# Kernel tuning notes

Hardware: AMD Instinct MI355X
Metric: run time of the kernel (lower is better)

## Reference

```python
import jax, jax.numpy as jnp
import numpy as np

B, S, D, H = 4, 2048, 512, 8
DK = D // H
SCALE = 1.0 / np.sqrt(DK)


def setup_inputs() -> dict:
    key = jax.random.key(0)
    kx, kq, kk, kv = jax.random.split(key, 4)
    w_std = np.sqrt(2.0 / (D + D))  # xavier-ish scale
    return {
        "x": jax.random.normal(kx, (B, S, D), dtype=jnp.float32),
        "W_Q": jax.random.normal(kq, (D, D), dtype=jnp.float32) * w_std,
        "W_K": jax.random.normal(kk, (D, D), dtype=jnp.float32) * w_std,
        "W_V": jax.random.normal(kv, (D, D), dtype=jnp.float32) * w_std,
    }


def reference(x, W_Q, W_K, W_V):
    # torch Linear(bias=False): y = x @ W.T
    q = jnp.einsum('bsd,ed->bse', x, W_Q).reshape(B, S, H, DK).transpose(0, 2, 1, 3)
    k = jnp.einsum('bsd,ed->bse', x, W_K).reshape(B, S, H, DK).transpose(0, 2, 1, 3)
    v = jnp.einsum('bsd,ed->bse', x, W_V).reshape(B, S, H, DK).transpose(0, 2, 1, 3)
    scores = jnp.einsum('bhqd,bhkd->bhqk', q, k) * SCALE  # [B,H,S,S]
    scores_exp = jnp.exp(scores)  # faithful: no max-subtraction in original
    attn = scores_exp / (scores_exp.sum(axis=-1, keepdims=True) + 1e-8)
    context = jnp.einsum('bhqk,bhkd->bhqd', attn, v)
    return context.transpose(0, 2, 1, 3).reshape(B, S, D)
```

## Files before the change

### kernel.cpp

```cpp
#include <hip/hip_runtime.h>
#include <hip/hip_bf16.h>

#define Bsz 4
#define Ssz 2048
#define Dsz 512
#define Hsz 8
#define DKsz 64

typedef __bf16 bf16x8 __attribute__((ext_vector_type(8)));
typedef float f32x4 __attribute__((ext_vector_type(4)));

__global__ __launch_bounds__(256) void cvt_kernel(
    const float* __restrict__ x, const float* __restrict__ Wq,
    const float* __restrict__ Wk, const float* __restrict__ Wv,
    __bf16* __restrict__ xb, __bf16* __restrict__ Wb)
{
    const int i = blockIdx.x * 256 + threadIdx.x;
    const int XN4 = (Bsz * Ssz * Dsz) / 4;
    const float* src;
    __bf16* dst;
    int off;
    if (i < XN4) {
        src = x; dst = xb; off = i;
    } else {
        int j = i - XN4;
        int w = j >> 16;
        off = j & 65535;
        src = (w == 0) ? Wq : (w == 1) ? Wk : Wv;
        dst = Wb + (size_t)w * (Dsz * Dsz);
    }
    float4 v = ((const float4*)src)[off];
    __bf16 o[4] = {(__bf16)v.x, (__bf16)v.y, (__bf16)v.z, (__bf16)v.w};
    *(uint2*)(dst + (size_t)off * 4) = *(uint2*)o;
}

__global__ __launch_bounds__(256) void qkv_proj_kernel(
    const __bf16* __restrict__ xb, const __bf16* __restrict__ Wb,
    __bf16* __restrict__ Qo, __bf16* __restrict__ Ko, __bf16* __restrict__ Vo)
{
    __shared__ __bf16 xs[128][72];
    __shared__ __bf16 wsh[128][72];

    const int tid  = threadIdx.x;
    const int lane = tid & 63;
    const int wave = tid >> 6;
    const int quad = lane >> 4;
    const int l16  = lane & 15;
    const int wm   = (wave & 1) * 64;
    const int wn   = (wave >> 1) * 64;

    const int tm = blockIdx.x * 128;
    const int tn = blockIdx.y * 128;
    const int which = blockIdx.z;
    const __bf16* W = Wb + (size_t)which * (Dsz * Dsz);

    const int srow = tid >> 1;
    const int scol = (tid & 1) * 32;

    f32x4 acc[4][4];
    #pragma unroll
    for (int i = 0; i < 4; ++i)
        #pragma unroll
        for (int j = 0; j < 4; ++j) acc[i][j] = (f32x4){0.f, 0.f, 0.f, 0.f};

    const __bf16* xrow = xb + (size_t)(tm + srow) * Dsz + scol;
    const __bf16* wrow = W  + (size_t)(tn + srow) * Dsz + scol;

    bf16x8 px[4], pw[4];
    #pragma unroll
    for (int i = 0; i < 4; ++i) {
        px[i] = *(const bf16x8*)(xrow + 8 * i);
        pw[i] = *(const bf16x8*)(wrow + 8 * i);
    }

    const __bf16 (*Ash)[72] = (which == 2) ? wsh : xs;
    const __bf16 (*Bsh)[72] = (which == 2) ? xs : wsh;

    for (int k0 = 0; k0 < Dsz; k0 += 64) {
        __syncthreads();
        #pragma unroll
        for (int i = 0; i < 4; ++i) {
            *(bf16x8*)&xs[srow][scol + 8 * i]  = px[i];
            *(bf16x8*)&wsh[srow][scol + 8 * i] = pw[i];
        }
        __syncthreads();
        if (k0 + 64 < Dsz) {
            #pragma unroll
            for (int i = 0; i < 4; ++i) {
                px[i] = *(const bf16x8*)(xrow + k0 + 64 + 8 * i);
                pw[i] = *(const bf16x8*)(wrow + k0 + 64 + 8 * i);
            }
        }

        #pragma unroll
        for (int kk = 0; kk < 2; ++kk) {
            bf16x8 a[4], b[4];
            #pragma unroll
            for (int mi = 0; mi < 4; ++mi)
                a[mi] = *(const bf16x8*)&Ash[wm + mi * 16 + l16][kk * 32 + quad * 8];
            #pragma unroll
            for (int ni = 0; ni < 4; ++ni)
                b[ni] = *(const bf16x8*)&Bsh[wn + ni * 16 + l16][kk * 32 + quad * 8];
            #pragma unroll
            for (int mi = 0; mi < 4; ++mi)
                #pragma unroll
                for (int ni = 0; ni < 4; ++ni)
                    acc[mi][ni] = __builtin_amdgcn_mfma_f32_16x16x32_bf16(
                        a[mi], b[ni], acc[mi][ni], 0, 0, 0);
        }
    }

    const float qscale = 0.125f * 1.44269504088896340736f;

    if (which != 2) {
        #pragma unroll
        for (int ni = 0; ni < 4; ++ni) {
            const int n = tn + wn + ni * 16 + l16;
            const int h = n >> 6, d = n & 63;
            #pragma unroll
            for (int mi = 0; mi < 4; ++mi) {
                #pragma unroll
                for (int r = 0; r < 4; ++r) {
                    const int m = tm + wm + mi * 16 + quad * 4 + r;
                    const int b = m >> 11, s = m & (Ssz - 1);
                    const float v = acc[mi][ni][r];
                    if (which == 0)
                        Qo[((((size_t)b * Hsz + h) * Ssz + s) << 6) + d] = (__bf16)(v * qscale);
                    else
                        Ko[((((size_t)b * Hsz + h) * Ssz + s) << 6) + d] = (__bf16)v;
                }
            }
        }
    } else {
        #pragma unroll
        for (int mi = 0; mi < 4; ++mi) {
            #pragma unroll
            for (int r = 0; r < 4; ++r) {
                const int e = tn + wm + mi * 16 + quad * 4 + r;
                const int h = e >> 6, d = e & 63;
                #pragma unroll
                for (int ni = 0; ni < 4; ++ni) {
                    const int sx = tm + wn + ni * 16 + l16;
                    const int b = sx >> 11, s = sx & (Ssz - 1);
                    Vo[(((size_t)b * Hsz + h) * DKsz + d) * Ssz + s] = (__bf16)acc[mi][ni][r];
                }
            }
        }
    }
}

__global__ __launch_bounds__(256, 2) void attn_kernel(
    const __bf16* __restrict__ Q, const __bf16* __restrict__ K,
    const __bf16* __restrict__ VT, float* __restrict__ out)
{
    __shared__ __bf16 ks[64][72];
    __shared__ __bf16 vs[64][72];
    __shared__ __bf16 ps[4][2][16][72];

    const int tid  = threadIdx.x;
    const int lane = tid & 63;
    const int wave = tid >> 6;
    const int quad = lane >> 4;
    const int l16  = lane & 15;

    const int bh = blockIdx.x;
    const int qt = blockIdx.y;
    const int b  = bh >> 3;
    const int h  = bh & 7;

    const __bf16* Qb = Q  + (size_t)bh * Ssz * DKsz;
    const __bf16* Kb = K  + (size_t)bh * Ssz * DKsz;
    const __bf16* Vb = VT + (size_t)bh * DKsz * Ssz;

    bf16x8 qf[2][2];
    #pragma unroll
    for (int qs = 0; qs < 2; ++qs) {
        const __bf16* qrow = Qb + (size_t)(qt * 128 + qs * 64 + wave * 16 + l16) * DKsz;
        qf[qs][0] = *(const bf16x8*)(qrow + quad * 8);
        qf[qs][1] = *(const bf16x8*)(qrow + 32 + quad * 8);
    }

    bf16x8 ones;
    #pragma unroll
    for (int i = 0; i < 8; ++i) ones[i] = (__bf16)1.0f;

    f32x4 oacc[2][4];
    #pragma unroll
    for (int qs = 0; qs < 2; ++qs)
        #pragma unroll
        for (int i = 0; i < 4; ++i) oacc[qs][i] = (f32x4){0.f, 0.f, 0.f, 0.f};
    f32x4 lacc[2] = {(f32x4){0.f, 0.f, 0.f, 0.f}, (f32x4){0.f, 0.f, 0.f, 0.f}};

    const int srow = tid >> 2;
    const int sc   = (tid & 3) * 8;

    const __bf16* krow = Kb + (size_t)srow * DKsz + sc;
    const __bf16* vrow = Vb + (size_t)srow * Ssz + sc;

    bf16x8 pk0 = *(const bf16x8*)(krow);
    bf16x8 pk1 = *(const bf16x8*)(krow + 32);
    bf16x8 pv0 = *(const bf16x8*)(vrow);
    bf16x8 pv1 = *(const bf16x8*)(vrow + 32);

    for (int kb = 0; kb < Ssz; kb += 64) {
        __syncthreads();
        *(bf16x8*)&ks[srow][sc]      = pk0;
        *(bf16x8*)&ks[srow][32 + sc] = pk1;
        *(bf16x8*)&vs[srow][sc]      = pv0;
        *(bf16x8*)&vs[srow][32 + sc] = pv1;
        __syncthreads();

        if (kb + 64 < Ssz) {
            pk0 = *(const bf16x8*)(krow + (size_t)(kb + 64) * DKsz);
            pk1 = *(const bf16x8*)(krow + (size_t)(kb + 64) * DKsz + 32);
            pv0 = *(const bf16x8*)(vrow + kb + 64);
            pv1 = *(const bf16x8*)(vrow + kb + 96);
        }

        bf16x8 kf[2][4], vf[2][4];
        #pragma unroll
        for (int kk = 0; kk < 2; ++kk)
            #pragma unroll
            for (int ns = 0; ns < 4; ++ns) {
                kf[kk][ns] = *(const bf16x8*)&ks[ns * 16 + l16][kk * 32 + quad * 8];
                vf[kk][ns] = *(const bf16x8*)&vs[ns * 16 + l16][kk * 32 + quad * 8];
            }

        #pragma unroll
        for (int qs = 0; qs < 2; ++qs) {
            f32x4 sacc[4];
            #pragma unroll
            for (int ns = 0; ns < 4; ++ns) {
                sacc[ns] = (f32x4){0.f, 0.f, 0.f, 0.f};
                sacc[ns] = __builtin_amdgcn_mfma_f32_16x16x32_bf16(qf[qs][0], kf[0][ns], sacc[ns], 0, 0, 0);
                sacc[ns] = __builtin_amdgcn_mfma_f32_16x16x32_bf16(qf[qs][1], kf[1][ns], sacc[ns], 0, 0, 0);
            }
            #pragma unroll
            for (int ns = 0; ns < 4; ++ns)
                #pragma unroll
                for (int r = 0; r < 4; ++r)
                    ps[wave][qs][quad * 4 + r][ns * 16 + l16] =
                        (__bf16)__builtin_amdgcn_exp2f(sacc[ns][r]);

            bf16x8 af0 = *(const bf16x8*)&ps[wave][qs][l16][quad * 8];
            bf16x8 af1 = *(const bf16x8*)&ps[wave][qs][l16][32 + quad * 8];
            #pragma unroll
            for (int ns = 0; ns < 4; ++ns) {
                oacc[qs][ns] = __builtin_amdgcn_mfma_f32_16x16x32_bf16(af0, vf[0][ns], oacc[qs][ns], 0, 0, 0);
                oacc[qs][ns] = __builtin_amdgcn_mfma_f32_16x16x32_bf16(af1, vf[1][ns], oacc[qs][ns], 0, 0, 0);
            }
            lacc[qs] = __builtin_amdgcn_mfma_f32_16x16x32_bf16(af0, ones, lacc[qs], 0, 0, 0);
            lacc[qs] = __builtin_amdgcn_mfma_f32_16x16x32_bf16(af1, ones, lacc[qs], 0, 0, 0);
        }
    }

    #pragma unroll
    for (int qs = 0; qs < 2; ++qs) {
        float linv[4];
        #pragma unroll
        for (int r = 0; r < 4; ++r) linv[r] = 1.f / (lacc[qs][r] + 1e-8f);
        #pragma unroll
        for (int ns = 0; ns < 4; ++ns) {
            const int d = ns * 16 + l16;
            #pragma unroll
            for (int r = 0; r < 4; ++r) {
                const int s = qt * 128 + qs * 64 + wave * 16 + quad * 4 + r;
                out[((size_t)b * Ssz + s) * Dsz + h * DKsz + d] = oacc[qs][ns][r] * linv[r];
            }
        }
    }
}

extern "C" void kernel_launch(void* const* d_in, const int* in_sizes, int n_in,
                              void* d_out, int out_size, void* d_ws, size_t ws_size,
                              hipStream_t stream) {
    const float* x  = (const float*)d_in[0];
    const float* Wq = (const float*)d_in[1];
    const float* Wk = (const float*)d_in[2];
    const float* Wv = (const float*)d_in[3];
    float* out = (float*)d_out;

    const size_t per = (size_t)Bsz * Hsz * Ssz * DKsz;
    __bf16* Qw  = (__bf16*)d_ws;
    __bf16* Kw  = Qw + per;
    __bf16* VTw = Kw + per;
    __bf16* xb  = VTw + per;
    __bf16* Wb  = xb + per;

    cvt_kernel<<<4864, 256, 0, stream>>>(x, Wq, Wk, Wv, xb, Wb);
    qkv_proj_kernel<<<dim3((Bsz * Ssz) / 128, Dsz / 128, 3), 256, 0, stream>>>(
        xb, Wb, Qw, Kw, VTw);
    attn_kernel<<<dim3(Bsz * Hsz, Ssz / 128), 256, 0, stream>>>(Qw, Kw, VTw, out);
}
```

Measured before the change: 152.2 us.

## Swizzle LDS, split QKV projection by operand order, enlarge attention query tile

LDS tiles in both the projection and attention kernels drop their row padding and use an XOR swizzle to avoid bank conflicts. The QKV projection is split into a Q/K kernel and a V kernel via a template, with operand order chosen so results can be written as 4-wide bf16 vector stores. The attention kernel now processes 256 queries per block (64 per wave), reusing each K/V tile for twice as many queries. It also swaps the MFMA operands so the output tile is transposed, which lets the fp32 output be written with 16-byte vector stores. The trade-off is that the attention grid halves to 256 blocks at one block per CU, leaving fewer waves to hide latency, and register pressure rises.

```diff
diff --git a/kernel.cpp b/kernel.cpp
--- a/kernel.cpp
+++ b/kernel.cpp
@@ -8,7 +8,10 @@
 #define DKsz 64
 
 typedef __bf16 bf16x8 __attribute__((ext_vector_type(8)));
+typedef __bf16 bf16x4 __attribute__((ext_vector_type(4)));
 typedef float f32x4 __attribute__((ext_vector_type(4)));
+
+#define SWE(c, row) ((((c) ^ ((row) & 7)) * 8))
 
 __global__ __launch_bounds__(256) void cvt_kernel(
     const float* __restrict__ x, const float* __restrict__ Wq,
@@ -34,12 +37,13 @@
     *(uint2*)(dst + (size_t)off * 4) = *(uint2*)o;
 }
 
-__global__ __launch_bounds__(256) void qkv_proj_kernel(
-    const __bf16* __restrict__ xb, const __bf16* __restrict__ Wb,
-    __bf16* __restrict__ Qo, __bf16* __restrict__ Ko, __bf16* __restrict__ Vo)
-{
-    __shared__ __bf16 xs[128][72];
-    __shared__ __bf16 wsh[128][72];
+template<bool VM>
+__device__ __forceinline__ void qkv_body(
+    const __bf16* __restrict__ xb, const __bf16* __restrict__ W,
+    __bf16* __restrict__ dst, float scale)
+{
+    __shared__ __bf16 xs[128][64];
+    __shared__ __bf16 wsh[128][64];
 
     const int tid  = threadIdx.x;
     const int lane = tid & 63;
@@ -51,111 +55,123 @@
 
     const int tm = blockIdx.x * 128;
     const int tn = blockIdx.y * 128;
-    const int which = blockIdx.z;
-    const __bf16* W = Wb + (size_t)which * (Dsz * Dsz);
 
     const int srow = tid >> 1;
-    const int scol = (tid & 1) * 32;
+    const int c0   = (tid & 1) * 4;
+
+    const __bf16* xg = xb + (size_t)(tm + srow) * Dsz;
+    const __bf16* wg = W  + (size_t)(tn + srow) * Dsz;
+
+    bf16x8 px[4], pw[4];
+    #pragma unroll
+    for (int i = 0; i < 4; ++i) {
+        px[i] = *(const bf16x8*)(xg + (c0 + i) * 8);
+        pw[i] = *(const bf16x8*)(wg + (c0 + i) * 8);
+    }
 
     f32x4 acc[4][4];
     #pragma unroll
     for (int i = 0; i < 4; ++i)
         #pragma unroll
         for (int j = 0; j < 4; ++j) acc[i][j] = (f32x4){0.f, 0.f, 0.f, 0.f};
-
-    const __bf16* xrow = xb + (size_t)(tm + srow) * Dsz + scol;
-    const __bf16* wrow = W  + (size_t)(tn + srow) * Dsz + scol;
-
-    bf16x8 px[4], pw[4];
-    #pragma unroll
-    for (int i = 0; i < 4; ++i) {
-        px[i] = *(const bf16x8*)(xrow + 8 * i);
-        pw[i] = *(const bf16x8*)(wrow + 8 * i);
-    }
-
-    const __bf16 (*Ash)[72] = (which == 2) ? wsh : xs;
-    const __bf16 (*Bsh)[72] = (which == 2) ? xs : wsh;
 
     for (int k0 = 0; k0 < Dsz; k0 += 64) {
         __syncthreads();
         #pragma unroll
         for (int i = 0; i < 4; ++i) {
-            *(bf16x8*)&xs[srow][scol + 8 * i]  = px[i];
-            *(bf16x8*)&wsh[srow][scol + 8 * i] = pw[i];
+            *(bf16x8*)&xs[srow][SWE(c0 + i, srow)]  = px[i];
+            *(bf16x8*)&wsh[srow][SWE(c0 + i, srow)] = pw[i];
         }
         __syncthreads();
         if (k0 + 64 < Dsz) {
             #pragma unroll
             for (int i = 0; i < 4; ++i) {
-                px[i] = *(const bf16x8*)(xrow + k0 + 64 + 8 * i);
-                pw[i] = *(const bf16x8*)(wrow + k0 + 64 + 8 * i);
+                px[i] = *(const bf16x8*)(xg + k0 + 64 + (c0 + i) * 8);
+                pw[i] = *(const bf16x8*)(wg + k0 + 64 + (c0 + i) * 8);
             }
         }
 
         #pragma unroll
         for (int kk = 0; kk < 2; ++kk) {
-            bf16x8 a[4], b[4];
-            #pragma unroll
-            for (int mi = 0; mi < 4; ++mi)
-                a[mi] = *(const bf16x8*)&Ash[wm + mi * 16 + l16][kk * 32 + quad * 8];
-            #pragma unroll
-            for (int ni = 0; ni < 4; ++ni)
-                b[ni] = *(const bf16x8*)&Bsh[wn + ni * 16 + l16][kk * 32 + quad * 8];
+            bf16x8 fa[4], fb[4];
+            #pragma unroll
+            for (int mi = 0; mi < 4; ++mi) {
+                const int row = wm + mi * 16 + l16;
+                fa[mi] = VM ? *(const bf16x8*)&xs[row][SWE(kk * 4 + quad, row)]
+                            : *(const bf16x8*)&wsh[row][SWE(kk * 4 + quad, row)];
+            }
+            #pragma unroll
+            for (int ni = 0; ni < 4; ++ni) {
+                const int row = wn + ni * 16 + l16;
+                fb[ni] = VM ? *(const bf16x8*)&wsh[row][SWE(kk * 4 + quad, row)]
+                            : *(const bf16x8*)&xs[row][SWE(kk * 4 + quad, row)];
+            }
             #pragma unroll
             for (int mi = 0; mi < 4; ++mi)
                 #pragma unroll
                 for (int ni = 0; ni < 4; ++ni)
                     acc[mi][ni] = __builtin_amdgcn_mfma_f32_16x16x32_bf16(
-                        a[mi], b[ni], acc[mi][ni], 0, 0, 0);
-        }
-    }
-
+                        fa[mi], fb[ni], acc[mi][ni], 0, 0, 0);
+        }
+    }
+
+    if (!VM) {
+        #pragma unroll
+        for (int mi = 0; mi < 4; ++mi) {
+            const int e0 = tn + wm + mi * 16 + quad * 4;
+            const int h = e0 >> 6, d0 = e0 & 63;
+            #pragma unroll
+            for (int ni = 0; ni < 4; ++ni) {
+                const int sf = tm + wn + ni * 16 + l16;
+                const int b = sf >> 11, s = sf & (Ssz - 1);
+                bf16x4 p;
+                #pragma unroll
+                for (int r = 0; r < 4; ++r) p[r] = (__bf16)(acc[mi][ni][r] * scale);
+                *(bf16x4*)&dst[((((size_t)(b * Hsz + h) * Ssz + s)) << 6) + d0] = p;
+            }
+        }
+    } else {
+        #pragma unroll
+        for (int mi = 0; mi < 4; ++mi) {
+            const int sf0 = tm + wm + mi * 16 + quad * 4;
+            const int b = sf0 >> 11, s0 = sf0 & (Ssz - 1);
+            #pragma unroll
+            for (int ni = 0; ni < 4; ++ni) {
+                const int e = tn + wn + ni * 16 + l16;
+                const int h = e >> 6, d = e & 63;
+                bf16x4 p;
+                #pragma unroll
+                for (int r = 0; r < 4; ++r) p[r] = (__bf16)acc[mi][ni][r];
+                *(bf16x4*)&dst[(((size_t)(b * Hsz + h) * DKsz + d) << 11) + s0] = p;
+            }
+        }
+    }
+}
+
+__global__ __launch_bounds__(256, 2) void qkv_qk_kernel(
+    const __bf16* __restrict__ xb, const __bf16* __restrict__ Wb,
+    __bf16* __restrict__ Qo, __bf16* __restrict__ Ko)
+{
+    const int which = blockIdx.z;
     const float qscale = 0.125f * 1.44269504088896340736f;
-
-    if (which != 2) {
-        #pragma unroll
-        for (int ni = 0; ni < 4; ++ni) {
-            const int n = tn + wn + ni * 16 + l16;
-            const int h = n >> 6, d = n & 63;
-            #pragma unroll
-            for (int mi = 0; mi < 4; ++mi) {
-                #pragma unroll
-                for (int r = 0; r < 4; ++r) {
-                    const int m = tm + wm + mi * 16 + quad * 4 + r;
-                    const int b = m >> 11, s = m & (Ssz - 1);
-                    const float v = acc[mi][ni][r];
-                    if (which == 0)
-                        Qo[((((size_t)b * Hsz + h) * Ssz + s) << 6) + d] = (__bf16)(v * qscale);
-                    else
-                        Ko[((((size_t)b * Hsz + h) * Ssz + s) << 6) + d] = (__bf16)v;
-                }
-            }
-        }
-    } else {
-        #pragma unroll
-        for (int mi = 0; mi < 4; ++mi) {
-            #pragma unroll
-            for (int r = 0; r < 4; ++r) {
-                const int e = tn + wm + mi * 16 + quad * 4 + r;
-                const int h = e >> 6, d = e & 63;
-                #pragma unroll
-                for (int ni = 0; ni < 4; ++ni) {
-                    const int sx = tm + wn + ni * 16 + l16;
-                    const int b = sx >> 11, s = sx & (Ssz - 1);
-                    Vo[(((size_t)b * Hsz + h) * DKsz + d) * Ssz + s] = (__bf16)acc[mi][ni][r];
-                }
-            }
-        }
-    }
-}
-
-__global__ __launch_bounds__(256, 2) void attn_kernel(
+    qkv_body<false>(xb, Wb + (size_t)which * (Dsz * Dsz),
+                    which == 0 ? Qo : Ko, which == 0 ? qscale : 1.0f);
+}
+
+__global__ __launch_bounds__(256, 2) void qkv_v_kernel(
+    const __bf16* __restrict__ xb, const __bf16* __restrict__ Wb,
+    __bf16* __restrict__ Vo)
+{
+    qkv_body<true>(xb, Wb + (size_t)2 * (Dsz * Dsz), Vo, 1.0f);
+}
+
+__global__ __launch_bounds__(256, 1) void attn_kernel(
     const __bf16* __restrict__ Q, const __bf16* __restrict__ K,
     const __bf16* __restrict__ VT, float* __restrict__ out)
 {
-    __shared__ __bf16 ks[64][72];
-    __shared__ __bf16 vs[64][72];
-    __shared__ __bf16 ps[4][2][16][72];
+    __shared__ __bf16 ks[64][64];
+    __shared__ __bf16 vs[64][64];
+    __shared__ __bf16 ps[4][16][64];
 
     const int tid  = threadIdx.x;
     const int lane = tid & 63;
@@ -172,10 +188,10 @@
     const __bf16* Kb = K  + (size_t)bh * Ssz * DKsz;
     const __bf16* Vb = VT + (size_t)bh * DKsz * Ssz;
 
-    bf16x8 qf[2][2];
-    #pragma unroll
-    for (int qs = 0; qs < 2; ++qs) {
-        const __bf16* qrow = Qb + (size_t)(qt * 128 + qs * 64 + wave * 16 + l16) * DKsz;
+    bf16x8 qf[4][2];
+    #pragma unroll
+    for (int qs = 0; qs < 4; ++qs) {
+        const __bf16* qrow = Qb + (size_t)(qt * 256 + wave * 64 + qs * 16 + l16) * DKsz;
         qf[qs][0] = *(const bf16x8*)(qrow + quad * 8);
         qf[qs][1] = *(const bf16x8*)(qrow + 32 + quad * 8);
     }
@@ -184,37 +200,36 @@
     #pragma unroll
     for (int i = 0; i < 8; ++i) ones[i] = (__bf16)1.0f;
 
-    f32x4 oacc[2][4];
-    #pragma unroll
-    for (int qs = 0; qs < 2; ++qs)
+    f32x4 oacc[4][4];
+    #pragma unroll
+    for (int qs = 0; qs < 4; ++qs)
         #pragma unroll
         for (int i = 0; i < 4; ++i) oacc[qs][i] = (f32x4){0.f, 0.f, 0.f, 0.f};
-    f32x4 lacc[2] = {(f32x4){0.f, 0.f, 0.f, 0.f}, (f32x4){0.f, 0.f, 0.f, 0.f}};
+    f32x4 lacc[4];
+    #pragma unroll
+    for (int qs = 0; qs < 4; ++qs) lacc[qs] = (f32x4){0.f, 0.f, 0.f, 0.f};
 
     const int srow = tid >> 2;
-    const int sc   = (tid & 3) * 8;
-
-    const __bf16* krow = Kb + (size_t)srow * DKsz + sc;
-    const __bf16* vrow = Vb + (size_t)srow * Ssz + sc;
-
-    bf16x8 pk0 = *(const bf16x8*)(krow);
-    bf16x8 pk1 = *(const bf16x8*)(krow + 32);
-    bf16x8 pv0 = *(const bf16x8*)(vrow);
-    bf16x8 pv1 = *(const bf16x8*)(vrow + 32);
+    const int c0   = tid & 3;
+
+    bf16x8 pk0 = *(const bf16x8*)(Kb + (size_t)srow * DKsz + c0 * 8);
+    bf16x8 pk1 = *(const bf16x8*)(Kb + (size_t)srow * DKsz + (c0 + 4) * 8);
+    bf16x8 pv0 = *(const bf16x8*)(Vb + (size_t)srow * Ssz + c0 * 8);
+    bf16x8 pv1 = *(const bf16x8*)(Vb + (size_t)srow * Ssz + (c0 + 4) * 8);
 
     for (int kb = 0; kb < Ssz; kb += 64) {
         __syncthreads();
-        *(bf16x8*)&ks[srow][sc]      = pk0;
-        *(bf16x8*)&ks[srow][32 + sc] = pk1;
-        *(bf16x8*)&vs[srow][sc]      = pv0;
-        *(bf16x8*)&vs[srow][32 + sc] = pv1;
+        *(bf16x8*)&ks[srow][SWE(c0, srow)]     = pk0;
+        *(bf16x8*)&ks[srow][SWE(c0 + 4, srow)] = pk1;
+        *(bf16x8*)&vs[srow][SWE(c0, srow)]     = pv0;
+        *(bf16x8*)&vs[srow][SWE(c0 + 4, srow)] = pv1;
         __syncthreads();
 
         if (kb + 64 < Ssz) {
-            pk0 = *(const bf16x8*)(krow + (size_t)(kb + 64) * DKsz);
-            pk1 = *(const bf16x8*)(krow + (size_t)(kb + 64) * DKsz + 32);
-            pv0 = *(const bf16x8*)(vrow + kb + 64);
-            pv1 = *(const bf16x8*)(vrow + kb + 96);
+            pk0 = *(const bf16x8*)(Kb + (size_t)(kb + 64 + srow) * DKsz + c0 * 8);
+            pk1 = *(const bf16x8*)(Kb + (size_t)(kb + 64 + srow) * DKsz + (c0 + 4) * 8);
+            pv0 = *(const bf16x8*)(Vb + (size_t)srow * Ssz + kb + 64 + c0 * 8);
+            pv1 = *(const bf16x8*)(Vb + (size_t)srow * Ssz + kb + 64 + (c0 + 4) * 8);
         }
 
         bf16x8 kf[2][4], vf[2][4];
@@ -222,12 +237,13 @@
         for (int kk = 0; kk < 2; ++kk)
             #pragma unroll
             for (int ns = 0; ns < 4; ++ns) {
-                kf[kk][ns] = *(const bf16x8*)&ks[ns * 16 + l16][kk * 32 + quad * 8];
-                vf[kk][ns] = *(const bf16x8*)&vs[ns * 16 + l16][kk * 32 + quad * 8];
-            }
-
-        #pragma unroll
-        for (int qs = 0; qs < 2; ++qs) {
+                const int row = ns * 16 + l16;
+                kf[kk][ns] = *(const bf16x8*)&ks[row][SWE(kk * 4 + quad, row)];
+                vf[kk][ns] = *(const bf16x8*)&vs[row][SWE(kk * 4 + quad, row)];
+            }
+
+        #pragma unroll
+        for (int qs = 0; qs < 4; ++qs) {
             f32x4 sacc[4];
             #pragma unroll
             for (int ns = 0; ns < 4; ++ns) {
@@ -236,37 +252,36 @@
                 sacc[ns] = __builtin_amdgcn_mfma_f32_16x16x32_bf16(qf[qs][1], kf[1][ns], sacc[ns], 0, 0, 0);
             }
             #pragma unroll
-            for (int ns = 0; ns < 4; ++ns)
+            for (int ns = 0; ns < 4; ++ns) {
+                const int c = ns * 2 + (l16 >> 3);
                 #pragma unroll
-                for (int r = 0; r < 4; ++r)
-                    ps[wave][qs][quad * 4 + r][ns * 16 + l16] =
+                for (int r = 0; r < 4; ++r) {
+                    const int prow = quad * 4 + r;
+                    ps[wave][prow][SWE(c, prow) + (l16 & 7)] =
                         (__bf16)__builtin_amdgcn_exp2f(sacc[ns][r]);
-
-            bf16x8 af0 = *(const bf16x8*)&ps[wave][qs][l16][quad * 8];
-            bf16x8 af1 = *(const bf16x8*)&ps[wave][qs][l16][32 + quad * 8];
+                }
+            }
+            bf16x8 af0 = *(const bf16x8*)&ps[wave][l16][SWE(quad, l16)];
+            bf16x8 af1 = *(const bf16x8*)&ps[wave][l16][SWE(4 + quad, l16)];
             #pragma unroll
             for (int ns = 0; ns < 4; ++ns) {
-                oacc[qs][ns] = __builtin_amdgcn_mfma_f32_16x16x32_bf16(af0, vf[0][ns], oacc[qs][ns], 0, 0, 0);
-                oacc[qs][ns] = __builtin_amdgcn_mfma_f32_16x16x32_bf16(af1, vf[1][ns], oacc[qs][ns], 0, 0, 0);
-            }
-            lacc[qs] = __builtin_amdgcn_mfma_f32_16x16x32_bf16(af0, ones, lacc[qs], 0, 0, 0);
-            lacc[qs] = __builtin_amdgcn_mfma_f32_16x16x32_bf16(af1, ones, lacc[qs], 0, 0, 0);
-        }
-    }
-
-    #pragma unroll
-    for (int qs = 0; qs < 2; ++qs) {
-        float linv[4];
-        #pragma unroll
-        for (int r = 0; r < 4; ++r) linv[r] = 1.f / (lacc[qs][r] + 1e-8f);
+                oacc[qs][ns] = __builtin_amdgcn_mfma_f32_16x16x32_bf16(vf[0][ns], af0, oacc[qs][ns], 0, 0, 0);
+                oacc[qs][ns] = __builtin_amdgcn_mfma_f32_16x16x32_bf16(vf[1][ns], af1, oacc[qs][ns], 0, 0, 0);
+            }
+            lacc[qs] = __builtin_amdgcn_mfma_f32_16x16x32_bf16(ones, af0, lacc[qs], 0, 0, 0);
+            lacc[qs] = __builtin_amdgcn_mfma_f32_16x16x32_bf16(ones, af1, lacc[qs], 0, 0, 0);
+        }
+    }
+
+    #pragma unroll
+    for (int qs = 0; qs < 4; ++qs) {
+        const float linv = 1.f / (lacc[qs][0] + 1e-8f);
+        const int q = qt * 256 + wave * 64 + qs * 16 + l16;
+        float* obase = out + ((size_t)b * Ssz + q) * Dsz + h * DKsz;
         #pragma unroll
         for (int ns = 0; ns < 4; ++ns) {
-            const int d = ns * 16 + l16;
-            #pragma unroll
-            for (int r = 0; r < 4; ++r) {
-                const int s = qt * 128 + qs * 64 + wave * 16 + quad * 4 + r;
-                out[((size_t)b * Ssz + s) * Dsz + h * DKsz + d] = oacc[qs][ns][r] * linv[r];
-            }
+            f32x4 o = oacc[qs][ns] * linv;
+            *(f32x4*)(obase + ns * 16 + quad * 4) = o;
         }
     }
 }
@@ -288,7 +303,7 @@
     __bf16* Wb  = xb + per;
 
     cvt_kernel<<<4864, 256, 0, stream>>>(x, Wq, Wk, Wv, xb, Wb);
-    qkv_proj_kernel<<<dim3((Bsz * Ssz) / 128, Dsz / 128, 3), 256, 0, stream>>>(
-        xb, Wb, Qw, Kw, VTw);
-    attn_kernel<<<dim3(Bsz * Hsz, Ssz / 128), 256, 0, stream>>>(Qw, Kw, VTw, out);
-}
+    qkv_qk_kernel<<<dim3((Bsz * Ssz) / 128, Dsz / 128, 2), 256, 0, stream>>>(xb, Wb, Qw, Kw);
+    qkv_v_kernel<<<dim3((Bsz * Ssz) / 128, Dsz / 128), 256, 0, stream>>>(xb, Wb, VTw);
+    attn_kernel<<<dim3(Bsz * Hsz, Ssz / 256), 256, 0, stream>>>(Qw, Kw, VTw, out);
+}
```

Measured after the change: 162.7 us. 1.07x slower.
